# Optimization experiments

Hardware: AMD Instinct MI355X
Metric: run time of the kernel (lower is better)

## Reference

```python
import jax, jax.numpy as jnp
import numpy as np

N_NODES = 100000
N_EDGES = 600000
N_GRAPHS = 256
K = 5
N_FEAT = 16
N_CLASSES = 4


def setup_inputs() -> dict:
    key = jax.random.key(0)
    ks = jax.random.split(key, 12)
    x = jax.random.normal(ks[0], (N_NODES, N_FEAT), dtype=jnp.float32)
    edge_index = jax.random.randint(ks[1], (2, N_EDGES), 0, N_NODES, dtype=jnp.int32)
    batch = jnp.sort(jax.random.randint(ks[2], (N_NODES,), 0, N_GRAPHS, dtype=jnp.int32))
    s = 0.1
    W11 = jax.random.normal(ks[3], (K, N_FEAT, 64), dtype=jnp.float32) * s
    b11 = jnp.zeros((64,), dtype=jnp.float32)
    W12 = jax.random.normal(ks[4], (K, N_FEAT, 64), dtype=jnp.float32) * s
    b12 = jnp.zeros((64,), dtype=jnp.float32)
    W21 = jax.random.normal(ks[5], (K, 128, 256), dtype=jnp.float32) * s
    b21 = jnp.zeros((256,), dtype=jnp.float32)
    W22 = jax.random.normal(ks[6], (K, 128, 256), dtype=jnp.float32) * s
    b22 = jnp.zeros((256,), dtype=jnp.float32)
    fc_w = jax.random.normal(ks[7], (512, N_CLASSES), dtype=jnp.float32) * s
    fc_b = jnp.zeros((N_CLASSES,), dtype=jnp.float32)
    return {
        "x": x, "edge_index": edge_index, "batch": batch,
        "W11": W11, "b11": b11, "W12": W12, "b12": b12,
        "W21": W21, "b21": b21, "W22": W22, "b22": b22,
        "fc_w": fc_w, "fc_b": fc_b,
    }


def _cheb_norm(src, dst, n_nodes):
    # PyG ChebConv (sym norm, lambda_max=2): L_hat = -D^{-1/2} A D^{-1/2},
    # zero diagonal. Degree computed over source (row) indices.
    deg = jax.ops.segment_sum(jnp.ones_like(src, dtype=jnp.float32), src,
                              num_segments=n_nodes)
    dinv = jnp.where(deg > 0, jax.lax.rsqrt(jnp.maximum(deg, 1.0)), 0.0)
    return -dinv[src] * dinv[dst]


def _cheb_conv(x, src, dst, w_norm, W, b):
    # Chebyshev recursion: Tx0=x, Tx1=L_hat x, Txk = 2 L_hat Tx_{k-1} - Tx_{k-2}
    n = x.shape[0]

    def spmm(h):  # aggregate messages from src at dst
        return jax.ops.segment_sum(h[src] * w_norm[:, None], dst, num_segments=n)

    Tx0 = x
    Tx1 = spmm(x)
    out = jnp.einsum('nf,fo->no', Tx0, W[0]) + jnp.einsum('nf,fo->no', Tx1, W[1])
    for k in range(2, W.shape[0]):
        Tx2 = 2.0 * spmm(Tx1) - Tx0
        out = out + jnp.einsum('nf,fo->no', Tx2, W[k])
        Tx0, Tx1 = Tx1, Tx2
    return out + b


def reference(x, edge_index, batch, W11, b11, W12, b12, W21, b21, W22, b22,
              fc_w, fc_b):
    src, dst = edge_index[0], edge_index[1]
    w_fwd = _cheb_norm(src, dst, N_NODES)
    w_rev = _cheb_norm(dst, src, N_NODES)  # reversed adjacency

    x1 = jax.nn.relu(_cheb_conv(x, src, dst, w_fwd, W11, b11))
    x2 = jax.nn.relu(_cheb_conv(x, dst, src, w_rev, W12, b12))
    h = jnp.concatenate([x1, x2], axis=1)  # [N, 128]

    x1 = jax.nn.relu(_cheb_conv(h, src, dst, w_fwd, W21, b21))
    x2 = jax.nn.relu(_cheb_conv(h, dst, src, w_rev, W22, b22))
    h = jnp.concatenate([x1, x2], axis=1)  # [N, 512]

    # global mean pool over graphs
    sums = jax.ops.segment_sum(h, batch, num_segments=N_GRAPHS)
    cnt = jax.ops.segment_sum(jnp.ones((h.shape[0],), dtype=h.dtype), batch,
                              num_segments=N_GRAPHS)
    pooled = sums / jnp.maximum(cnt, 1.0)[:, None]  # [G, 512]

    logits = pooled @ fc_w + fc_b
    return jax.nn.log_softmax(logits, axis=1)
```

## Files before the change

kernel.cpp:

```cpp
#include <hip/hip_runtime.h>
#include <stdint.h>

#define NNODES 100000
#define NEDGES 600000
#define NGRAPH 256
#define KCH 5
#define F1 16
#define O1 64
#define F2 128
#define O2 256
#define FT1 (KCH * F1)
#define FT2 (KCH * F2)
#define KSTEPS 20
#define KS1 3
#define NXCD 8

typedef unsigned short ushort_t;
typedef __attribute__((ext_vector_type(8))) short bf16x8;
typedef __attribute__((ext_vector_type(4))) float f32x4;

__device__ __forceinline__ float bflo(unsigned int u) {
    union { unsigned int u; float f; } v; v.u = u << 16; return v.f;
}
__device__ __forceinline__ float bfhi(unsigned int u) {
    union { unsigned int u; float f; } v; v.u = u & 0xFFFF0000u; return v.f;
}
__device__ __forceinline__ unsigned int f2bf(float f) {
    union { float f; unsigned int u; } v; v.f = f;
    return (v.u + 0x7FFFu + ((v.u >> 16) & 1u)) >> 16;
}
__device__ __forceinline__ unsigned int pack2(float lo, float hi) {
    return (f2bf(hi) << 16) | f2bf(lo);
}


__global__ void k_count(const int* __restrict__ src, const int* __restrict__ dst,
                        int* __restrict__ cntDst, int* __restrict__ cntSrc, int E) {
    int e = blockIdx.x * 256 + threadIdx.x;
    if (e < E) {
        atomicAdd(&cntDst[dst[e]], 1);
        atomicAdd(&cntSrc[src[e]], 1);
    }
}

__global__ void k_dinv(const int* __restrict__ cntDst, const int* __restrict__ cntSrc,
                       float* __restrict__ dinvF, float* __restrict__ dinvR, int n) {
    int i = blockIdx.x * 256 + threadIdx.x;
    if (i < n) {
        int cs = cntSrc[i], cd = cntDst[i];
        dinvF[i] = cs > 0 ? rsqrtf((float)cs) : 0.f;
        dinvR[i] = cd > 0 ? rsqrtf((float)cd) : 0.f;
    }
}

__global__ void k_scan1(const int* __restrict__ in, int* __restrict__ out,
                        int* __restrict__ blksum, int n) {
    __shared__ int a[512];
    __shared__ int s[256];
    int t = threadIdx.x;
    int base = blockIdx.x * 512;
    a[t]       = (base + t < n)       ? in[base + t]       : 0;
    a[t + 256] = (base + t + 256 < n) ? in[base + t + 256] : 0;
    __syncthreads();
    s[t] = a[2 * t] + a[2 * t + 1];
    __syncthreads();
    for (int off = 1; off < 256; off <<= 1) {
        int v = (t >= off) ? s[t - off] : 0;
        __syncthreads();
        s[t] += v;
        __syncthreads();
    }
    int ep = (t > 0) ? s[t - 1] : 0;
    if (base + 2 * t < n)     out[base + 2 * t]     = ep;
    if (base + 2 * t + 1 < n) out[base + 2 * t + 1] = ep + a[2 * t];
    if (t == 255) blksum[blockIdx.x] = s[255];
}

__global__ void k_scan2(int* __restrict__ blksum, int nb) {
    __shared__ int s[256];
    int t = threadIdx.x;
    s[t] = (t < nb) ? blksum[t] : 0;
    __syncthreads();
    for (int off = 1; off < 256; off <<= 1) {
        int v = (t >= off) ? s[t - off] : 0;
        __syncthreads();
        s[t] += v;
        __syncthreads();
    }
    if (t < nb) blksum[t] = (t > 0) ? s[t - 1] : 0;
}

__global__ void k_scan3(int* __restrict__ out, const int* __restrict__ blksum, int n) {
    int i = blockIdx.x * 512 + threadIdx.x;
    int add = blksum[blockIdx.x];
    if (i < n) out[i] += add;
    if (i + 256 < n) out[i + 256] += add;
}

__global__ void k_tail(int* __restrict__ off_f, int* __restrict__ off_r, int n, int E) {
    if (threadIdx.x == 0) { off_f[n] = E; off_r[n] = E; }
}

__global__ void k_scatter(const int* __restrict__ src, const int* __restrict__ dst,
                          const float* __restrict__ dinvF, const float* __restrict__ dinvR,
                          int* __restrict__ curF, int* __restrict__ curR,
                          int2* __restrict__ edF, int2* __restrict__ edR, int E,
                          int chunk) {
    int c = blockIdx.x & (NXCD - 1);
    int sb = blockIdx.x >> 3;
    int slices = gridDim.x >> 3;
    int lo = c * chunk, hi = lo + chunk;
    for (int e = sb * 256 + threadIdx.x; e < E; e += slices * 256) {
        int s = src[e], d = dst[e];
        if (d >= lo && d < hi) {
            int p = atomicAdd(&curF[d], 1);
            float wf = -dinvF[s] * dinvF[d];
            edF[p] = make_int2(s, __float_as_int(wf));
        }
        if (s >= lo && s < hi) {
            int q = atomicAdd(&curR[s], 1);
            float wr = -dinvR[s] * dinvR[d];
            edR[q] = make_int2(d, __float_as_int(wr));
        }
    }
}

__global__ void k_gstart(const int* __restrict__ batch, int* __restrict__ gstart, int n) {
    int g = blockIdx.x * 64 + threadIdx.x;
    if (g > NGRAPH) return;
    if (g == NGRAPH) { gstart[g] = n; return; }
    int lo = 0, hi = n;
    while (lo < hi) {
        int mid = (lo + hi) >> 1;
        if (batch[mid] < g) lo = mid + 1; else hi = mid;
    }
    gstart[g] = lo;
}


__global__ void k_copyx(const float* __restrict__ x, float* __restrict__ Tx, int n) {
    int tid = blockIdx.x * 256 + threadIdx.x;
    int r = tid >> 2, c = tid & 3;
    if (r < n)
        *(float4*)(Tx + (size_t)r * FT1 + c * 4) =
            *(const float4*)(x + (size_t)r * 16 + c * 4);
}

__global__ void k_spmm_f32(const float* __restrict__ Hin, float* __restrict__ Hout,
                           const float* __restrict__ Tx0,
                           const int* __restrict__ off, const int2* __restrict__ ed,
                           int n) {
    int tid = blockIdx.x * 256 + threadIdx.x;
    int r = tid >> 2, c = tid & 3;
    if (r >= n) return;
    int j0 = off[r], j1 = off[r + 1];
    float4 s = {0.f, 0.f, 0.f, 0.f};
    int j = j0;
    for (; j + 4 <= j1; j += 4) {
        int2 e0 = ed[j], e1 = ed[j + 1], e2 = ed[j + 2], e3 = ed[j + 3];
        float wa = __int_as_float(e0.y), wb = __int_as_float(e1.y);
        float wc = __int_as_float(e2.y), wd = __int_as_float(e3.y);
        const float4 h0 = *(const float4*)(Hin + (size_t)e0.x * FT1 + c * 4);
        const float4 h1 = *(const float4*)(Hin + (size_t)e1.x * FT1 + c * 4);
        const float4 h2 = *(const float4*)(Hin + (size_t)e2.x * FT1 + c * 4);
        const float4 h3 = *(const float4*)(Hin + (size_t)e3.x * FT1 + c * 4);
        s.x += wa * h0.x; s.y += wa * h0.y; s.z += wa * h0.z; s.w += wa * h0.w;
        s.x += wb * h1.x; s.y += wb * h1.y; s.z += wb * h1.z; s.w += wb * h1.w;
        s.x += wc * h2.x; s.y += wc * h2.y; s.z += wc * h2.z; s.w += wc * h2.w;
        s.x += wd * h3.x; s.y += wd * h3.y; s.z += wd * h3.z; s.w += wd * h3.w;
    }
    for (; j < j1; ++j) {
        int2 e = ed[j];
        float w2 = __int_as_float(e.y);
        const float4 h = *(const float4*)(Hin + (size_t)e.x * FT1 + c * 4);
        s.x += w2 * h.x; s.y += w2 * h.y; s.z += w2 * h.z; s.w += w2 * h.w;
    }
    float4 o;
    if (Tx0) {
        const float4 t0 = *(const float4*)(Tx0 + (size_t)r * FT1 + c * 4);
        o.x = 2.f * s.x - t0.x; o.y = 2.f * s.y - t0.y;
        o.z = 2.f * s.z - t0.z; o.w = 2.f * s.w - t0.w;
    } else {
        o = s;
    }
    *(float4*)(Hout + (size_t)r * FT1 + c * 4) = o;
}

__global__ void k_spmm_bf(const ushort_t* __restrict__ Hin, ushort_t* __restrict__ Hout,
                          const ushort_t* __restrict__ Tx0,
                          const int* __restrict__ off, const int2* __restrict__ ed,
                          int n) {
    int r = blockIdx.x * 4 + (threadIdx.x >> 6);
    r = __builtin_amdgcn_readfirstlane(r);
    int c = threadIdx.x & 63;
    if (r >= n) return;
    int j0 = __builtin_amdgcn_readfirstlane(off[r]);
    int j1 = __builtin_amdgcn_readfirstlane(off[r + 1]);
    float s0 = 0.f, s1 = 0.f;
    int j = j0;
    int jfull = j0 + ((j1 - j0) & ~7);
    for (; j < jfull; j += 8) {
        float w[8];
        unsigned int h[8];
#pragma unroll
        for (int sl = 0; sl < 8; ++sl) {
            int2 e = ed[j + sl];
            w[sl] = __int_as_float(e.y);
            h[sl] = *(const unsigned int*)(Hin + (size_t)e.x * FT2 + c * 2);
        }
#pragma unroll
        for (int sl = 0; sl < 8; ++sl) {
            s0 = fmaf(bflo(h[sl]), w[sl], s0);
            s1 = fmaf(bfhi(h[sl]), w[sl], s1);
        }
    }
    int rem = j1 - j;
    if (rem) {
        float w[8];
        unsigned int h[8];
#pragma unroll
        for (int sl = 0; sl < 8; ++sl) {
            w[sl] = 0.f; h[sl] = 0u;
            if (sl < rem) {
                int2 e = ed[j + sl];
                w[sl] = __int_as_float(e.y);
                h[sl] = *(const unsigned int*)(Hin + (size_t)e.x * FT2 + c * 2);
            }
        }
#pragma unroll
        for (int sl = 0; sl < 8; ++sl) {
            s0 = fmaf(bflo(h[sl]), w[sl], s0);
            s1 = fmaf(bfhi(h[sl]), w[sl], s1);
        }
    }
    if (Tx0) {
        unsigned int t0 = *(const unsigned int*)(Tx0 + (size_t)r * FT2 + c * 2);
        s0 = 2.f * s0 - bflo(t0);
        s1 = 2.f * s1 - bfhi(t0);
    }
    *(unsigned int*)(Hout + (size_t)r * FT2 + c * 2) = pack2(s0, s1);
}

__global__ void k_packW1(const float* __restrict__ W, ushort_t* __restrict__ Bp) {
    int tid = blockIdx.x * 256 + threadIdx.x;
    if (tid >= 4 * KS1 * 64) return;
    int lane = tid & 63;
    int ks = (tid >> 6) % KS1;
    int nt = tid / (64 * KS1);
    int k0 = ks * 32 + (lane >> 4) * 8;
    int ncol = nt * 16 + (lane & 15);
    float v[8];
#pragma unroll
    for (int j = 0; j < 8; ++j) {
        int k = k0 + j;
        v[j] = (k < FT1) ? W[(size_t)k * O1 + ncol] : 0.f;
    }
    uint4 o;
    o.x = pack2(v[0], v[1]); o.y = pack2(v[2], v[3]);
    o.z = pack2(v[4], v[5]); o.w = pack2(v[6], v[7]);
    *(uint4*)(Bp + (size_t)tid * 8) = o;
}

__global__ __launch_bounds__(256) void k_gemm1_mfma(
    const float* __restrict__ A, const ushort_t* __restrict__ Bp,
    const float* __restrict__ bias, ushort_t* __restrict__ out, int n) {
    int lane = threadIdx.x & 63;
    int wvi = threadIdx.x >> 6;
    int mrow = lane & 15;
    int quad = lane >> 4;
    int m0w = blockIdx.x * 64 + wvi * 16;
    int row = m0w + mrow;
    int rowc = row < n ? row : n - 1;
    const float* Ar = A + (size_t)rowc * FT1 + quad * 8;

    f32x4 acc[4] = {};
#pragma unroll
    for (int ks = 0; ks < KS1; ++ks) {
        float4 a0 = *(const float4*)(Ar + ks * 32);
        float4 a1 = *(const float4*)(Ar + ks * 32 + 4);
        union { bf16x8 v; unsigned int u[4]; } ua;
        ua.u[0] = pack2(a0.x, a0.y);
        ua.u[1] = pack2(a0.z, a0.w);
        ua.u[2] = pack2(a1.x, a1.y);
        ua.u[3] = pack2(a1.z, a1.w);
#pragma unroll
        for (int nf = 0; nf < 4; ++nf) {
            bf16x8 bfr = *(const bf16x8*)(Bp + ((size_t)(nf * KS1 + ks) * 64 + lane) * 8);
            acc[nf] = __builtin_amdgcn_mfma_f32_16x16x32_bf16(ua.v, bfr, acc[nf], 0, 0, 0);
        }
    }
#pragma unroll
    for (int nf = 0; nf < 4; ++nf) {
        float bb = bias[nf * 16 + mrow];
#pragma unroll
        for (int reg = 0; reg < 4; ++reg) {
            int orow = m0w + quad * 4 + reg;
            if (orow < n)
                out[(size_t)orow * FT2 + nf * 16 + mrow] =
                    (ushort_t)f2bf(fmaxf(acc[nf][reg] + bb, 0.f));
        }
    }
}

__global__ void k_packW(const float* __restrict__ W, ushort_t* __restrict__ Bp) {
    int tid = blockIdx.x * 256 + threadIdx.x;
    if (tid >= 16 * KSTEPS * 64) return;
    int lane = tid & 63;
    int ks = (tid >> 6) % KSTEPS;
    int nt = tid / (64 * KSTEPS);
    int k0 = ks * 32 + (lane >> 4) * 8;
    int ncol = nt * 16 + (lane & 15);
    float v[8];
#pragma unroll
    for (int j = 0; j < 8; ++j) v[j] = W[(size_t)(k0 + j) * O2 + ncol];
    uint4 o;
    o.x = pack2(v[0], v[1]); o.y = pack2(v[2], v[3]);
    o.z = pack2(v[4], v[5]); o.w = pack2(v[6], v[7]);
    *(uint4*)(Bp + (size_t)tid * 8) = o;
}

__global__ __launch_bounds__(256) void k_gemm2_mfma(
    const ushort_t* __restrict__ A, const ushort_t* __restrict__ Bp,
    const float* __restrict__ bias, float* __restrict__ pooled, int colofs,
    const int* __restrict__ batch, int n) {
    int lane = threadIdx.x & 63;
    int wv = threadIdx.x >> 6;
    int m0 = blockIdx.x * 64;
    int mrow = lane & 15;
    int quad = lane >> 4;

    const ushort_t* Abase[4];
#pragma unroll
    for (int mf = 0; mf < 4; ++mf) {
        int row = m0 + mf * 16 + mrow;
        int rowc = row < n ? row : n - 1;
        Abase[mf] = A + (size_t)rowc * FT2 + quad * 8;
    }
    const ushort_t* Bbase = Bp + ((size_t)(wv * 4) * KSTEPS * 64 + lane) * 8;

    f32x4 acc[4][4] = {};
    bf16x8 acur[4], bcur[4], anxt[4], bnxt[4];
#pragma unroll
    for (int mf = 0; mf < 4; ++mf) acur[mf] = *(const bf16x8*)(Abase[mf]);
#pragma unroll
    for (int nf = 0; nf < 4; ++nf)
        bcur[nf] = *(const bf16x8*)(Bbase + ((size_t)nf * KSTEPS) * 512);

#pragma unroll 2
    for (int ks = 0; ks < KSTEPS; ++ks) {
        if (ks + 1 < KSTEPS) {
#pragma unroll
            for (int mf = 0; mf < 4; ++mf)
                anxt[mf] = *(const bf16x8*)(Abase[mf] + (ks + 1) * 32);
#pragma unroll
            for (int nf = 0; nf < 4; ++nf)
                bnxt[nf] = *(const bf16x8*)(Bbase + ((size_t)nf * KSTEPS + ks + 1) * 512);
        }
#pragma unroll
        for (int mf = 0; mf < 4; ++mf)
#pragma unroll
            for (int nf = 0; nf < 4; ++nf)
                acc[mf][nf] = __builtin_amdgcn_mfma_f32_16x16x32_bf16(
                    acur[mf], bcur[nf], acc[mf][nf], 0, 0, 0);
#pragma unroll
        for (int mf = 0; mf < 4; ++mf) acur[mf] = anxt[mf];
#pragma unroll
        for (int nf = 0; nf < 4; ++nf) bcur[nf] = bnxt[nf];
    }

    float bcol[4];
#pragma unroll
    for (int nf = 0; nf < 4; ++nf) bcol[nf] = bias[wv * 64 + nf * 16 + mrow];

#pragma unroll
    for (int mf = 0; mf < 4; ++mf) {
        int t0 = m0 + mf * 16;
        if (t0 >= n) break;
        int te = (t0 + 15 < n) ? t0 + 15 : n - 1;
        int r0 = t0 + quad * 4;
        if (batch[t0] == batch[te]) {
            int g = batch[t0];
#pragma unroll
            for (int nf = 0; nf < 4; ++nf) {
                float s = 0.f;
#pragma unroll
                for (int reg = 0; reg < 4; ++reg) {
                    float v = fmaxf(acc[mf][nf][reg] + bcol[nf], 0.f);
                    if (r0 + reg < n) s += v;
                }
                s += __shfl_xor(s, 16, 64);
                s += __shfl_xor(s, 32, 64);
                if (quad == 0)
                    atomicAdd(pooled + (size_t)g * 512 + colofs + wv * 64 + nf * 16 + mrow, s);
            }
        } else {
            int gb[4];
#pragma unroll
            for (int reg = 0; reg < 4; ++reg)
                gb[reg] = batch[(r0 + reg < n) ? r0 + reg : n - 1];
#pragma unroll
            for (int nf = 0; nf < 4; ++nf) {
                int col = colofs + wv * 64 + nf * 16 + mrow;
                float run = 0.f;
                int g = gb[0];
                bool any = false;
#pragma unroll
                for (int reg = 0; reg < 4; ++reg) {
                    int row = r0 + reg;
                    if (row >= n) break;
                    float v = fmaxf(acc[mf][nf][reg] + bcol[nf], 0.f);
                    if (gb[reg] != g) {
                        atomicAdd(pooled + (size_t)g * 512 + col, run);
                        run = 0.f;
                        g = gb[reg];
                    }
                    run += v;
                    any = true;
                }
                if (any) atomicAdd(pooled + (size_t)g * 512 + col, run);
            }
        }
    }
}

__global__ void k_logits(const float* __restrict__ pooled, const int* __restrict__ gstart,
                         const float* __restrict__ fcw, const float* __restrict__ fcb,
                         float* __restrict__ out) {
    int g = threadIdx.x;
    int cnt = gstart[g + 1] - gstart[g];
    float inv = 1.f / (float)(cnt > 1 ? cnt : 1);
    float lg[4];
#pragma unroll
    for (int o = 0; o < 4; ++o) lg[o] = fcb[o];
    for (int f = 0; f < 512; ++f) {
        float p = pooled[g * 512 + f] * inv;
#pragma unroll
        for (int o = 0; o < 4; ++o) lg[o] = fmaf(p, fcw[f * 4 + o], lg[o]);
    }
    float m = fmaxf(fmaxf(lg[0], lg[1]), fmaxf(lg[2], lg[3]));
    float s = 0.f;
#pragma unroll
    for (int o = 0; o < 4; ++o) s += expf(lg[o] - m);
    float l = logf(s);
#pragma unroll
    for (int o = 0; o < 4; ++o) out[g * 4 + o] = lg[o] - m - l;
}


extern "C" void kernel_launch(void* const* d_in, const int* in_sizes, int n_in,
                              void* d_out, int out_size, void* d_ws, size_t ws_size,
                              hipStream_t stream) {
    const float* x   = (const float*)d_in[0];
    const int* ei    = (const int*)d_in[1];
    const int* batch = (const int*)d_in[2];
    const float* W11 = (const float*)d_in[3];
    const float* b11 = (const float*)d_in[4];
    const float* W12 = (const float*)d_in[5];
    const float* b12 = (const float*)d_in[6];
    const float* W21 = (const float*)d_in[7];
    const float* b21 = (const float*)d_in[8];
    const float* W22 = (const float*)d_in[9];
    const float* b22 = (const float*)d_in[10];
    const float* fcw = (const float*)d_in[11];
    const float* fcb = (const float*)d_in[12];
    float* out = (float*)d_out;

    const int N = in_sizes[0] / F1;
    const int E = in_sizes[1] / 2;
    const int* src = ei;
    const int* dst = ei + E;

    char* w = (char*)d_ws;
    size_t pos = 0;
    auto alloc = [&](size_t bytes) -> void* {
        void* p = w + pos;
        pos += (bytes + 255) & ~(size_t)255;
        return p;
    };
    int* cur_f   = (int*)alloc((size_t)N * 4);
    int* cur_r   = (int*)alloc((size_t)N * 4);
    int* off_f   = (int*)alloc((size_t)(N + 1) * 4);
    int* off_r   = (int*)alloc((size_t)(N + 1) * 4);
    float* dinvF = (float*)alloc((size_t)N * 4);
    float* dinvR = (float*)alloc((size_t)N * 4);
    int2* ed_f   = (int2*)alloc((size_t)E * 8);
    int2* ed_r   = (int2*)alloc((size_t)E * 8);
    int* blks_f  = (int*)alloc(1024);
    int* blks_r  = (int*)alloc(1024);
    int* gstart  = (int*)alloc((NGRAPH + 1) * 4);
    float* pooled = (float*)alloc((size_t)NGRAPH * 512 * 4);
    ushort_t* BpF = (ushort_t*)alloc((size_t)FT2 * O2 * 2);
    ushort_t* BpR = (ushort_t*)alloc((size_t)FT2 * O2 * 2);
    ushort_t* Bp1F = (ushort_t*)alloc((size_t)4 * KS1 * 64 * 8 * 2);
    ushort_t* Bp1R = (ushort_t*)alloc((size_t)4 * KS1 * 64 * 8 * 2);
    float* TxAll1 = (float*)alloc(((size_t)N * FT1 + 256) * 4);
    ushort_t* TxAll2 = (ushort_t*)alloc((size_t)(N + 64) * FT2 * 2);

    (void)hipMemsetAsync(cur_f, 0, (size_t)N * 4, stream);
    (void)hipMemsetAsync(cur_r, 0, (size_t)N * 4, stream);
    (void)hipMemsetAsync(pooled, 0, (size_t)NGRAPH * 512 * 4, stream);

    int gE = (E + 255) / 256, gN = (N + 255) / 256;
    k_count<<<gE, 256, 0, stream>>>(src, dst, cur_f, cur_r, E);
    k_dinv<<<gN, 256, 0, stream>>>(cur_f, cur_r, dinvF, dinvR, N);

    int NB = (N + 511) / 512;
    k_scan1<<<NB, 256, 0, stream>>>(cur_f, off_f, blks_f, N);
    k_scan1<<<NB, 256, 0, stream>>>(cur_r, off_r, blks_r, N);
    k_scan2<<<1, 256, 0, stream>>>(blks_f, NB);
    k_scan2<<<1, 256, 0, stream>>>(blks_r, NB);
    k_scan3<<<NB, 256, 0, stream>>>(off_f, blks_f, N);
    k_scan3<<<NB, 256, 0, stream>>>(off_r, blks_r, N);
    k_tail<<<1, 64, 0, stream>>>(off_f, off_r, N, E);
    (void)hipMemcpyAsync(cur_f, off_f, (size_t)N * 4, hipMemcpyDeviceToDevice, stream);
    (void)hipMemcpyAsync(cur_r, off_r, (size_t)N * 4, hipMemcpyDeviceToDevice, stream);
    int chunk = (N + NXCD - 1) / NXCD;
    k_scatter<<<NXCD * 256, 256, 0, stream>>>(src, dst, dinvF, dinvR, cur_f, cur_r,
                                              ed_f, ed_r, E, chunk);
    k_gstart<<<5, 64, 0, stream>>>(batch, gstart, N);
    k_packW<<<80, 256, 0, stream>>>(W21, BpF);
    k_packW<<<80, 256, 0, stream>>>(W22, BpR);
    k_packW1<<<3, 256, 0, stream>>>(W11, Bp1F);
    k_packW1<<<3, 256, 0, stream>>>(W12, Bp1R);

    k_copyx<<<(N * 4 + 255) / 256, 256, 0, stream>>>(x, TxAll1, N);
    int gs1 = (N * 4 + 255) / 256;
    int gg1 = (N + 63) / 64;
    auto C1 = [&](int k) { return TxAll1 + k * F1; };
    k_spmm_f32<<<gs1, 256, 0, stream>>>(C1(0), C1(1), nullptr, off_f, ed_f, N);
    k_spmm_f32<<<gs1, 256, 0, stream>>>(C1(1), C1(2), C1(0), off_f, ed_f, N);
    k_spmm_f32<<<gs1, 256, 0, stream>>>(C1(2), C1(3), C1(1), off_f, ed_f, N);
    k_spmm_f32<<<gs1, 256, 0, stream>>>(C1(3), C1(4), C1(2), off_f, ed_f, N);
    k_gemm1_mfma<<<gg1, 256, 0, stream>>>(TxAll1, Bp1F, b11, TxAll2, N);
    k_spmm_f32<<<gs1, 256, 0, stream>>>(C1(0), C1(1), nullptr, off_r, ed_r, N);
    k_spmm_f32<<<gs1, 256, 0, stream>>>(C1(1), C1(2), C1(0), off_r, ed_r, N);
    k_spmm_f32<<<gs1, 256, 0, stream>>>(C1(2), C1(3), C1(1), off_r, ed_r, N);
    k_spmm_f32<<<gs1, 256, 0, stream>>>(C1(3), C1(4), C1(2), off_r, ed_r, N);
    k_gemm1_mfma<<<gg1, 256, 0, stream>>>(TxAll1, Bp1R, b12, TxAll2 + O1, N);

    int gs2 = (N + 3) / 4;
    auto C2 = [&](int k) { return TxAll2 + k * F2; };
    int gg = (N + 63) / 64;
    k_spmm_bf<<<gs2, 256, 0, stream>>>(C2(0), C2(1), nullptr, off_f, ed_f, N);
    k_spmm_bf<<<gs2, 256, 0, stream>>>(C2(1), C2(2), C2(0), off_f, ed_f, N);
    k_spmm_bf<<<gs2, 256, 0, stream>>>(C2(2), C2(3), C2(1), off_f, ed_f, N);
    k_spmm_bf<<<gs2, 256, 0, stream>>>(C2(3), C2(4), C2(2), off_f, ed_f, N);
    k_gemm2_mfma<<<gg, 256, 0, stream>>>(TxAll2, BpF, b21, pooled, 0, batch, N);
    k_spmm_bf<<<gs2, 256, 0, stream>>>(C2(0), C2(1), nullptr, off_r, ed_r, N);
    k_spmm_bf<<<gs2, 256, 0, stream>>>(C2(1), C2(2), C2(0), off_r, ed_r, N);
    k_spmm_bf<<<gs2, 256, 0, stream>>>(C2(2), C2(3), C2(1), off_r, ed_r, N);
    k_spmm_bf<<<gs2, 256, 0, stream>>>(C2(3), C2(4), C2(2), off_r, ed_r, N);
    k_gemm2_mfma<<<gg, 256, 0, stream>>>(TxAll2, BpR, b22, pooled, 256, batch, N);

    k_logits<<<1, 256, 0, stream>>>(pooled, gstart, fcw, fcb, out);
}
```

Before: 864.6 us.

## Stage GEMM2 A tiles in double-buffered LDS shared across waves

Result: faster. 788.8 us (-8.8%).

```diff
diff --git a/kernel.cpp b/kernel.cpp
--- a/kernel.cpp
+++ b/kernel.cpp
@@ -13,6 +13,8 @@
 #define FT2 (KCH * F2)
 #define KSTEPS 20
 #define KS1 3
+#define NBK 10
+#define LROW2 72
 #define NXCD 8
 
 typedef unsigned short ushort_t;
@@ -323,49 +325,64 @@
     const ushort_t* __restrict__ A, const ushort_t* __restrict__ Bp,
     const float* __restrict__ bias, float* __restrict__ pooled, int colofs,
     const int* __restrict__ batch, int n) {
+    __shared__ ushort_t lds[2][64 * LROW2];
+
     int lane = threadIdx.x & 63;
     int wv = threadIdx.x >> 6;
     int m0 = blockIdx.x * 64;
     int mrow = lane & 15;
     int quad = lane >> 4;
-
-    const ushort_t* Abase[4];
-#pragma unroll
-    for (int mf = 0; mf < 4; ++mf) {
-        int row = m0 + mf * 16 + mrow;
-        int rowc = row < n ? row : n - 1;
-        Abase[mf] = A + (size_t)rowc * FT2 + quad * 8;
-    }
+    int srow = threadIdx.x >> 2;
+    int sc = threadIdx.x & 3;
+
+    const ushort_t* Ag = A + (size_t)(m0 + srow) * FT2 + sc * 8;
     const ushort_t* Bbase = Bp + ((size_t)(wv * 4) * KSTEPS * 64 + lane) * 8;
+    int sidx = srow * LROW2 + sc * 8;
 
     f32x4 acc[4][4] = {};
-    bf16x8 acur[4], bcur[4], anxt[4], bnxt[4];
-#pragma unroll
-    for (int mf = 0; mf < 4; ++mf) acur[mf] = *(const bf16x8*)(Abase[mf]);
+    uint4 nxt0, nxt1;
+    bf16x8 bcur[4], bnxt[4];
+
+    *(uint4*)&lds[0][sidx]      = *(const uint4*)(Ag);
+    *(uint4*)&lds[0][sidx + 32] = *(const uint4*)(Ag + 32);
+    nxt0 = *(const uint4*)(Ag + 64);
+    nxt1 = *(const uint4*)(Ag + 96);
 #pragma unroll
     for (int nf = 0; nf < 4; ++nf)
         bcur[nf] = *(const bf16x8*)(Bbase + ((size_t)nf * KSTEPS) * 512);
 
-#pragma unroll 2
-    for (int ks = 0; ks < KSTEPS; ++ks) {
-        if (ks + 1 < KSTEPS) {
+    for (int bk = 0; bk < NBK; ++bk) {
+        __syncthreads();
+        if (bk + 1 < NBK) {
+            *(uint4*)&lds[(bk + 1) & 1][sidx]      = nxt0;
+            *(uint4*)&lds[(bk + 1) & 1][sidx + 32] = nxt1;
+        }
+        if (bk + 2 < NBK) {
+            nxt0 = *(const uint4*)(Ag + (bk + 2) * 64);
+            nxt1 = *(const uint4*)(Ag + (bk + 2) * 64 + 32);
+        }
+        const ushort_t* lbuf = &lds[bk & 1][0];
+#pragma unroll
+        for (int sub = 0; sub < 2; ++sub) {
+            int ks = bk * 2 + sub;
+            if (ks + 1 < KSTEPS) {
+#pragma unroll
+                for (int nf = 0; nf < 4; ++nf)
+                    bnxt[nf] = *(const bf16x8*)(Bbase + ((size_t)nf * KSTEPS + ks + 1) * 512);
+            }
+            bf16x8 af[4];
 #pragma unroll
             for (int mf = 0; mf < 4; ++mf)
-                anxt[mf] = *(const bf16x8*)(Abase[mf] + (ks + 1) * 32);
-#pragma unroll
-            for (int nf = 0; nf < 4; ++nf)
-                bnxt[nf] = *(const bf16x8*)(Bbase + ((size_t)nf * KSTEPS + ks + 1) * 512);
-        }
-#pragma unroll
-        for (int mf = 0; mf < 4; ++mf)
-#pragma unroll
-            for (int nf = 0; nf < 4; ++nf)
-                acc[mf][nf] = __builtin_amdgcn_mfma_f32_16x16x32_bf16(
-                    acur[mf], bcur[nf], acc[mf][nf], 0, 0, 0);
-#pragma unroll
-        for (int mf = 0; mf < 4; ++mf) acur[mf] = anxt[mf];
-#pragma unroll
-        for (int nf = 0; nf < 4; ++nf) bcur[nf] = bnxt[nf];
+                af[mf] = *(const bf16x8*)(lbuf + (mf * 16 + mrow) * LROW2 + sub * 32 + quad * 8);
+#pragma unroll
+            for (int mf = 0; mf < 4; ++mf)
+#pragma unroll
+                for (int nf = 0; nf < 4; ++nf)
+                    acc[mf][nf] = __builtin_amdgcn_mfma_f32_16x16x32_bf16(
+                        af[mf], bcur[nf], acc[mf][nf], 0, 0, 0);
+#pragma unroll
+            for (int nf = 0; nf < 4; ++nf) bcur[nf] = bnxt[nf];
+        }
     }
 
     float bcol[4];
```
